# Kernel tuning notes

Measured on AMD Instinct MI355X. Metric: run time of the kernel, lower is better.

Reference implementation:

```python
import jax, jax.numpy as jnp
import numpy as np
from jax.scipy.special import i0

IM_SIZE = (256, 256)
GRID_SIZE = (512, 512)
NUMPOINTS = 6
OS = GRID_SIZE[0] / IM_SIZE[0]
# Beatty et al. optimal Kaiser-Bessel shape parameter
BETA = float(np.pi * np.sqrt((NUMPOINTS / OS) ** 2 * (OS - 0.5) ** 2 - 0.8))


def _apod_1d(N, G):
    # 1/FT(kb kernel) scaling coefficients (de-apodization), static numpy
    x = np.arange(N) - N / 2.0
    arg = np.pi * NUMPOINTS * x / G
    t = BETA ** 2 - arg ** 2  # > 0 for this config
    ph = np.sinh(np.sqrt(t)) / np.sqrt(t)
    return (1.0 / ph).astype(np.float32)


def _kb(u):
    # Kaiser-Bessel interpolation kernel, support |u| <= NUMPOINTS/2
    x = 2.0 * u / NUMPOINTS
    t = 1.0 - x * x
    inside = t > 0
    t = jnp.where(inside, t, 0.0)
    return jnp.where(inside, i0(BETA * jnp.sqrt(t)), 0.0)


def setup_inputs():
    key = jax.random.key(0)
    k1, k2, k3 = jax.random.split(key, 3)
    B, M = 8, 131072
    image = jax.random.normal(k1, (B,) + IM_SIZE, dtype=jnp.float32)
    ktraj = (jax.random.uniform(k2, (B, 2, M), dtype=jnp.float32) * 2.0 - 1.0) * jnp.pi
    dcf = jax.random.uniform(k3, (B, M), dtype=jnp.float32)
    return {"image": image, "ktraj": ktraj, "dcf": dcf}


def _nufft(image, ktraj, dcf):
    B = image.shape[0]
    N1, N2 = IM_SIZE
    G1, G2 = GRID_SIZE
    J = NUMPOINTS
    # 1) de-apodization (scaling coefficients), separable per-dim
    a1 = jnp.asarray(_apod_1d(N1, G1))
    a2 = jnp.asarray(_apod_1d(N2, G2))
    img = image.astype(jnp.complex64) * (a1[:, None] * a2[None, :])
    # 2) centered zero-pad to oversampled grid, FFT with DC at bin 0
    p1, p2 = (G1 - N1) // 2, (G2 - N2) // 2
    grid = jnp.zeros((B, G1, G2), dtype=jnp.complex64).at[:, p1:p1 + N1, p2:p2 + N2].set(img)
    kgrid = jnp.fft.fft2(jnp.fft.ifftshift(grid, axes=(1, 2)))
    # 3) KB interpolation (gather) at non-uniform points
    tm1 = ktraj[:, 0] * (G1 / (2.0 * jnp.pi))  # (B,M) in grid units
    tm2 = ktraj[:, 1] * (G2 / (2.0 * jnp.pi))
    offs = jnp.arange(J, dtype=jnp.float32) - (J // 2 - 1)  # [-2..3]
    g1 = jnp.floor(tm1)[..., None] + offs  # (B,M,J) neighbor coords
    g2 = jnp.floor(tm2)[..., None] + offs
    w1 = _kb(tm1[..., None] - g1)
    w2 = _kb(tm2[..., None] - g2)
    i1 = jnp.mod(g1.astype(jnp.int32), G1)
    i2 = jnp.mod(g2.astype(jnp.int32), G2)
    lin = (i1[..., :, None] * G2 + i2[..., None, :]).reshape(B, -1)  # (B, M*J*J)
    vals = jnp.take_along_axis(kgrid.reshape(B, -1), lin, axis=1).reshape(B, -1, J, J)
    w = (w1[..., :, None] * w2[..., None, :]).astype(jnp.complex64)
    kdata = jnp.sum(vals * w, axis=(-1, -2))  # (B,M) complex
    kdata = kdata * dcf
    return jnp.stack([kdata.real, kdata.imag], axis=0)  # (2,B,M) float32


def reference(image, ktraj, dcf):
    return _nufft(image, ktraj, dcf)
```

## Files before the change

### kernel.cpp

```cpp
#include <hip/hip_runtime.h>
#include <math.h>

#define GSZ 512
#define NSZ 256
#define NBATCH 8
#define MPTS 131072
#define PI_F 3.14159265358979f
#define BETA_F 13.8551004f
#define BETA2_F (BETA_F * BETA_F)
#define RSQ2 0.70710678f
#define PADIDX(i) ((i) + ((i) >> 3))


__device__ __forceinline__ float apod(int i) {
    float x = (float)(i - 128);
    float arg = PI_F * 6.0f * x * (1.0f / 512.0f);
    float t = BETA2_F - arg * arg;
    float st = sqrtf(t);
    return st / sinhf(st);
}

__device__ __forceinline__ float kbw(float u) {
    float t = 1.0f - u * u * (1.0f / 9.0f);
    float x = BETA_F * sqrtf(fmaxf(t, 0.0f));
    float xc = fmaxf(x, 0.35f);
    float R = __builtin_amdgcn_rsqf(xc);
    float R2 = R * R;
    float q = R * (0.39894228f + R2 * (0.04986779f + R2 * 0.02804702f));
    float w = __expf(xc) * q;
    return (t > 0.0f) ? w : 0.0f;
}

template<int CTRL>
__device__ __forceinline__ float qdpp(float v) {
    int r = __builtin_amdgcn_mov_dpp(__float_as_int(v), CTRL, 0xF, 0xF, true);
    return __int_as_float(r);
}

struct __align__(8) F4 { float x, y, z, w; };

__device__ __forceinline__ float2 cadd(float2 a, float2 b){ return make_float2(a.x+b.x, a.y+b.y); }
__device__ __forceinline__ float2 csub(float2 a, float2 b){ return make_float2(a.x-b.x, a.y-b.y); }
__device__ __forceinline__ float2 cmul(float2 a, float2 b){ return make_float2(a.x*b.x-a.y*b.y, a.x*b.y+a.y*b.x); }
__device__ __forceinline__ float2 mul_negi(float2 a){ return make_float2(a.y, -a.x); }
__device__ __forceinline__ float2 mul_posi(float2 a){ return make_float2(-a.y, a.x); }
__device__ __forceinline__ float2 mul_w81(float2 a){ return make_float2(RSQ2*(a.x+a.y), RSQ2*(a.y-a.x)); }
__device__ __forceinline__ float2 mul_w83(float2 a){ return make_float2(RSQ2*(a.y-a.x), -RSQ2*(a.x+a.y)); }

__device__ __forceinline__ void dft8_combine(float2 E0, float2 E1, float2 E2, float2 E3,
                                             float2 O0, float2 O1, float2 O2, float2 O3,
                                             float2* y) {
    float2 c1 = mul_w81(O1), c2 = mul_negi(O2), c3 = mul_w83(O3);
    y[0] = cadd(E0, O0); y[4] = csub(E0, O0);
    y[1] = cadd(E1, c1); y[5] = csub(E1, c1);
    y[2] = cadd(E2, c2); y[6] = csub(E2, c2);
    y[3] = cadd(E3, c3); y[7] = csub(E3, c3);
}

__device__ __forceinline__ void dft8(const float2* x, float2* y) {
    float2 a0=x[0], a1=x[2], a2=x[4], a3=x[6];
    float2 b0=x[1], b1=x[3], b2=x[5], b3=x[7];
    float2 ta0=cadd(a0,a2), ta1=csub(a0,a2), ta2=cadd(a1,a3), ta3=csub(a1,a3);
    float2 E0=cadd(ta0,ta2), E2=csub(ta0,ta2);
    float2 E1=cadd(ta1, mul_negi(ta3)), E3=cadd(ta1, mul_posi(ta3));
    float2 tb0=cadd(b0,b2), tb1=csub(b0,b2), tb2=cadd(b1,b3), tb3=csub(b1,b3);
    float2 O0=cadd(tb0,tb2), O2=csub(tb0,tb2);
    float2 O1=cadd(tb1, mul_negi(tb3)), O3=cadd(tb1, mul_posi(tb3));
    dft8_combine(E0,E1,E2,E3,O0,O1,O2,O3,y);
}

__device__ __forceinline__ void dft8_pruned(float2 x0, float2 x1, float2 x6, float2 x7, float2* y) {
    float2 E0 = cadd(x0, x6), E2 = csub(x0, x6);
    float2 E1 = cadd(x0, mul_posi(x6)), E3 = cadd(x0, mul_negi(x6));
    float2 O0 = cadd(x1, x7), O2 = csub(x1, x7);
    float2 O1 = cadd(x1, mul_posi(x7)), O3 = cadd(x1, mul_negi(x7));
    dft8_combine(E0,E1,E2,E3,O0,O1,O2,O3,y);
}

template<int S>
__device__ __forceinline__ void twiddle8(int t, float2* y) {
    if (S < 2) {
        int j = (S == 0) ? t : (t >> 3);
        const float scale = (S == 0) ? (-2.0f*PI_F/512.0f) : (-2.0f*PI_F/64.0f);
        float theta = scale * (float)j;
        float sn, cs;
        __sincosf(theta, &sn, &cs);
        float2 w = make_float2(cs, sn), wq = w;
        y[1] = cmul(y[1], wq);
        #pragma unroll
        for (int q = 2; q < 8; ++q) { wq = cmul(wq, w); y[q] = cmul(y[q], wq); }
    }
}

__global__ __launch_bounds__(128) void pass1_rowfft(const float* __restrict__ image,
                                                    float2* __restrict__ T) {
    __shared__ float2 sm[2][2][578];
    int tid = threadIdx.x;
    int r = tid >> 6, t = tid & 63;
    int blk = blockIdx.x;
    int p = blk & 3;
    int g = blk >> 2;
    int rp = (g << 1) + r;
    int y = (rp < 128) ? rp : (rp + 256);
    int iy = (y < 128) ? (y + 128) : (y - 384);
    float ay = apod(iy);
    const float* irow0 = image + ((size_t)((2 * p)     * NSZ + iy)) * NSZ;
    const float* irow1 = image + ((size_t)((2 * p + 1) * NSZ + iy)) * NSZ;

    float2 y8[8];
    {
        int ix0 = t + 128, ix1 = t + 192, ix6 = t, ix7 = t + 64;
        float w0 = ay * apod(ix0), w1 = ay * apod(ix1);
        float w6 = ay * apod(ix6), w7 = ay * apod(ix7);
        float2 x0 = make_float2(irow0[ix0] * w0, irow1[ix0] * w0);
        float2 x1 = make_float2(irow0[ix1] * w1, irow1[ix1] * w1);
        float2 x6 = make_float2(irow0[ix6] * w6, irow1[ix6] * w6);
        float2 x7 = make_float2(irow0[ix7] * w7, irow1[ix7] * w7);
        dft8_pruned(x0, x1, x6, x7, y8);
        twiddle8<0>(t, y8);
    }
    float2* A  = sm[0][r];
    float2* Bf = sm[1][r];
    #pragma unroll
    for (int q = 0; q < 8; ++q) A[PADIDX((t << 3) + q)] = y8[q];
    __syncthreads();
    {
        float2 x[8];
        #pragma unroll
        for (int pp = 0; pp < 8; ++pp) x[pp] = A[PADIDX(t + (pp << 6))];
        dft8(x, y8);
        twiddle8<1>(t, y8);
        int j = t >> 3, k = t & 7, base = k + (j << 6);
        #pragma unroll
        for (int q = 0; q < 8; ++q) Bf[PADIDX(base + (q << 3))] = y8[q];
    }
    __syncthreads();
    {
        float2 x[8];
        #pragma unroll
        for (int pp = 0; pp < 8; ++pp) x[pp] = Bf[PADIDX(t + (pp << 6))];
        dft8(x, y8);
        float2* Trow = T + (((size_t)(p << 8) + rp) << 9);
        #pragma unroll
        for (int q = 0; q < 8; ++q) Trow[t + (q << 6)] = y8[q];
    }
}

__global__ __launch_bounds__(256) void pass2_colfft(const float2* __restrict__ T,
                                                    float2* __restrict__ kgrid) {
    __shared__ float2 B[8][578];
    int tid = threadIdx.x;
    int blk = blockIdx.x;
    int p = blk & 3;
    int g = blk >> 2;
    const float2* Tb = T + ((size_t)p << 17);
    float2* Kb0 = kgrid + ((size_t)(2 * p) << 18);
    float2* Kb1 = Kb0 + ((size_t)1 << 18);

    #define COLG(c) ((g > 0) ? (((c) < 4) ? ((g << 2) + (c)) : (505 - (g << 2) + (c))) \
                             : (((c) < 4) ? (c) : (((c) == 7) ? 256 : (505 + (c)))))

    {
        int c = tid & 7, r0 = tid >> 3;
        int colg = COLG(c);
        #pragma unroll
        for (int k = 0; k < 8; ++k) {
            int rr = r0 + (k << 5);
            B[c][PADIDX(rr)] = Tb[((size_t)rr << 9) + colg];
        }
    }
    __syncthreads();
    int t = tid & 63;
    int c0 = tid >> 6;
    float2* Ba = B[c0];
    float2* Bb = B[c0 + 4];
    float2 ya[8], yb[8];
    {
        float2 a0 = Ba[PADIDX(t)],       a1 = Ba[PADIDX(t + 64)];
        float2 a6 = Ba[PADIDX(t + 128)], a7 = Ba[PADIDX(t + 192)];
        float2 b0 = Bb[PADIDX(t)],       b1 = Bb[PADIDX(t + 64)];
        float2 b6 = Bb[PADIDX(t + 128)], b7 = Bb[PADIDX(t + 192)];
        dft8_pruned(a0, a1, a6, a7, ya); twiddle8<0>(t, ya);
        dft8_pruned(b0, b1, b6, b7, yb); twiddle8<0>(t, yb);
    }
    __syncthreads();
    #pragma unroll
    for (int q = 0; q < 8; ++q) {
        Ba[PADIDX((t << 3) + q)] = ya[q];
        Bb[PADIDX((t << 3) + q)] = yb[q];
    }
    __syncthreads();
    {
        float2 xa[8], xb[8];
        #pragma unroll
        for (int pp = 0; pp < 8; ++pp) { xa[pp] = Ba[PADIDX(t + (pp << 6))]; xb[pp] = Bb[PADIDX(t + (pp << 6))]; }
        dft8(xa, ya); twiddle8<1>(t, ya);
        dft8(xb, yb); twiddle8<1>(t, yb);
    }
    __syncthreads();
    {
        int j = t >> 3, k = t & 7, base = k + (j << 6);
        #pragma unroll
        for (int q = 0; q < 8; ++q) {
            Ba[PADIDX(base + (q << 3))] = ya[q];
            Bb[PADIDX(base + (q << 3))] = yb[q];
        }
    }
    __syncthreads();
    {
        float2 xa[8], xb[8];
        #pragma unroll
        for (int pp = 0; pp < 8; ++pp) { xa[pp] = Ba[PADIDX(t + (pp << 6))]; xb[pp] = Bb[PADIDX(t + (pp << 6))]; }
        dft8(xa, ya);
        dft8(xb, yb);
    }
    __syncthreads();
    #pragma unroll
    for (int q = 0; q < 8; ++q) {
        Ba[PADIDX(t + (q << 6))] = ya[q];
        Bb[PADIDX(t + (q << 6))] = yb[q];
    }
    __syncthreads();
    {
        int c = tid & 7, r0 = tid >> 3;
        int colg = COLG(c);
        int mc = 7 - c;
        if (g == 0) { if (c == 0) mc = 0; else if (c == 7) mc = 7; }
        #pragma unroll
        for (int k = 0; k < 16; ++k) {
            int rr = r0 + (k << 5);
            int mr = (512 - rr) & 511;
            float2 Z = B[c][PADIDX(rr)];
            float2 M = B[mc][PADIDX(mr)];
            float2 K0 = make_float2(0.5f * (Z.x + M.x), 0.5f * (Z.y - M.y));
            float2 K1 = make_float2(0.5f * (Z.y + M.y), 0.5f * (M.x - Z.x));
            size_t off = ((size_t)rr << 9) + colg;
            Kb0[off] = K0;
            Kb1[off] = K1;
        }
    }
    #undef COLG
}

__global__ __launch_bounds__(256) void interp_kb(const float* __restrict__ ktraj,
                                                 const float* __restrict__ dcf,
                                                 const float2* __restrict__ kgrid,
                                                 float* __restrict__ out) {
    int tid = threadIdx.x;
    int blk = blockIdx.x;
    int b = blk & 7;
    int gb = blk >> 3;
    int j = tid & 3;
    int q = tid >> 2;

    const float SCALE = (float)GSZ / (2.0f * PI_F);
    const float2* Kb = kgrid + ((size_t)b << 18);
    const float* kt1 = ktraj + ((size_t)(b * 2)) * MPTS;
    const float* kt2 = kt1 + MPTS;
    const float* dcfb = dcf + ((size_t)b << 17);
    float* out_re = out + ((size_t)b << 17);
    float* out_im = out_re + (size_t)NBATCH * MPTS;

    int m0 = (gb << 9) + q;
    float tm1 = kt1[m0] * SCALE;
    float tm2 = kt2[m0] * SCALE;
    float dd  = dcfb[m0];

    #pragma unroll 2
    for (int it = 0; it < 8; ++it) {
        int m = m0 + (it << 6);
        float f1 = floorf(tm1), f2 = floorf(tm2);
        int if1 = (int)f1, if2 = (int)f2;
        int e0 = (if2 - 2) & ~1;
        int cpair = (e0 + 2 * j) & 511;

        F4 v[6];
        #pragma unroll
        for (int a = 0; a < 6; ++a) {
            int rowb = (if1 + a - 2) & 511;
            v[a] = *reinterpret_cast<const F4*>(Kb + ((size_t)rowb << 9) + cpair);
        }

        float u2 = tm2 - (float)(e0 + 2 * j);
        float w2a = kbw(u2);
        float w2b = kbw(u2 - 1.0f);
        float fr1 = tm1 - f1;
        float w1A = kbw(fr1 - (float)(j - 2));
        float w1B = kbw(fr1 - (float)(j + 2));
        float w1_[6];
        w1_[0] = qdpp<0x00>(w1A);
        w1_[1] = qdpp<0x55>(w1A);
        w1_[2] = qdpp<0xAA>(w1A);
        w1_[3] = qdpp<0xFF>(w1A);
        w1_[4] = qdpp<0x00>(w1B);
        w1_[5] = qdpp<0x55>(w1B);
        float myd = dd;

        if (it < 7) {
            int mn = m + 64;
            tm1 = kt1[mn] * SCALE;
            tm2 = kt2[mn] * SCALE;
            dd  = dcfb[mn];
        }

        float c0re = 0.f, c0im = 0.f, c1re = 0.f, c1im = 0.f;
        #pragma unroll
        for (int a = 0; a < 6; ++a) {
            c0re = fmaf(w1_[a], v[a].x, c0re); c0im = fmaf(w1_[a], v[a].y, c0im);
            c1re = fmaf(w1_[a], v[a].z, c1re); c1im = fmaf(w1_[a], v[a].w, c1im);
        }
        float p_re = fmaf(w2a, c0re, w2b * c1re);
        float p_im = fmaf(w2a, c0im, w2b * c1im);
        p_re += qdpp<0xB1>(p_re);  p_re += qdpp<0x4E>(p_re);
        p_im += qdpp<0xB1>(p_im);  p_im += qdpp<0x4E>(p_im);

        if (j == 0) out_re[m] = p_re * myd;
        if (j == 1) out_im[m] = p_im * myd;
    }
}


extern "C" void kernel_launch(void* const* d_in, const int* in_sizes, int n_in,
                              void* d_out, int out_size, void* d_ws, size_t ws_size,
                              hipStream_t stream) {
    const float* image = (const float*)d_in[0];
    const float* ktraj = (const float*)d_in[1];
    const float* dcf   = (const float*)d_in[2];
    float* out = (float*)d_out;

    float2* T     = (float2*)d_ws;
    float2* kgrid = T + (size_t)4 * 256 * GSZ;

    pass1_rowfft<<<512, 128, 0, stream>>>(image, T);
    pass2_colfft<<<256, 256, 0, stream>>>(T, kgrid);
    interp_kb<<<NBATCH * 256, 256, 0, stream>>>(ktraj, dcf, kgrid, out);
}
```

Measured before the change: 128.4 us.

## Prefetch all trajectory inputs and double-buffer grid gathers in interpolation kernel

Result: slower. 132.1 us (+2.9%).

```diff
diff --git a/kernel.cpp b/kernel.cpp
--- a/kernel.cpp
+++ b/kernel.cpp
@@ -36,8 +36,6 @@
     int r = __builtin_amdgcn_mov_dpp(__float_as_int(v), CTRL, 0xF, 0xF, true);
     return __int_as_float(r);
 }
-
-struct __align__(8) F4 { float x, y, z, w; };
 
 __device__ __forceinline__ float2 cadd(float2 a, float2 b){ return make_float2(a.x+b.x, a.y+b.y); }
 __device__ __forceinline__ float2 csub(float2 a, float2 b){ return make_float2(a.x-b.x, a.y-b.y); }
@@ -252,9 +250,10 @@
     int gb = blk >> 3;
     int j = tid & 3;
     int q = tid >> 2;
+    int j2 = j << 1;
 
     const float SCALE = (float)GSZ / (2.0f * PI_F);
-    const float2* Kb = kgrid + ((size_t)b << 18);
+    const float* Kf = (const float*)(kgrid + ((size_t)b << 18));
     const float* kt1 = ktraj + ((size_t)(b * 2)) * MPTS;
     const float* kt2 = kt1 + MPTS;
     const float* dcfb = dcf + ((size_t)b << 17);
@@ -262,26 +261,32 @@
     float* out_im = out_re + (size_t)NBATCH * MPTS;
 
     int m0 = (gb << 9) + q;
-    float tm1 = kt1[m0] * SCALE;
-    float tm2 = kt2[m0] * SCALE;
-    float dd  = dcfb[m0];
-
-    #pragma unroll 2
+
+    float r1[8], r2[8], rd[8];
+    #pragma unroll
     for (int it = 0; it < 8; ++it) {
-        int m = m0 + (it << 6);
+        int mm = m0 + (it << 6);
+        r1[it] = __builtin_nontemporal_load(&kt1[mm]);
+        r2[it] = __builtin_nontemporal_load(&kt2[mm]);
+        rd[it] = __builtin_nontemporal_load(&dcfb[mm]);
+    }
+
+    auto issue = [&](float tm1, float tm2, float4* v, float& f1s, int& e0s) {
         float f1 = floorf(tm1), f2 = floorf(tm2);
         int if1 = (int)f1, if2 = (int)f2;
         int e0 = (if2 - 2) & ~1;
-        int cpair = (e0 + 2 * j) & 511;
-
-        F4 v[6];
+        int cpair = (e0 + j2) & 511;
         #pragma unroll
         for (int a = 0; a < 6; ++a) {
             int rowb = (if1 + a - 2) & 511;
-            v[a] = *reinterpret_cast<const F4*>(Kb + ((size_t)rowb << 9) + cpair);
-        }
-
-        float u2 = tm2 - (float)(e0 + 2 * j);
+            v[a] = *reinterpret_cast<const float4*>(Kf + ((rowb << 10) + (cpair << 1)));
+        }
+        f1s = f1; e0s = e0;
+    };
+
+    auto consume = [&](float tm1, float tm2, float f1, int e0, const float4* v,
+                       float dd, int m) {
+        float u2 = tm2 - (float)(e0 + j2);
         float w2a = kbw(u2);
         float w2b = kbw(u2 - 1.0f);
         float fr1 = tm1 - f1;
@@ -294,14 +299,6 @@
         w1_[3] = qdpp<0xFF>(w1A);
         w1_[4] = qdpp<0x00>(w1B);
         w1_[5] = qdpp<0x55>(w1B);
-        float myd = dd;
-
-        if (it < 7) {
-            int mn = m + 64;
-            tm1 = kt1[mn] * SCALE;
-            tm2 = kt2[mn] * SCALE;
-            dd  = dcfb[mn];
-        }
 
         float c0re = 0.f, c0im = 0.f, c1re = 0.f, c1im = 0.f;
         #pragma unroll
@@ -314,8 +311,30 @@
         p_re += qdpp<0xB1>(p_re);  p_re += qdpp<0x4E>(p_re);
         p_im += qdpp<0xB1>(p_im);  p_im += qdpp<0x4E>(p_im);
 
-        if (j == 0) out_re[m] = p_re * myd;
-        if (j == 1) out_im[m] = p_im * myd;
+        if (j == 0) __builtin_nontemporal_store(p_re * dd, &out_re[m]);
+        if (j == 1) __builtin_nontemporal_store(p_im * dd, &out_im[m]);
+    };
+
+    float4 vA[6], vB[6];
+    float f1A, f1B; int e0A, e0B;
+    float t1A = r1[0] * SCALE, t2A = r2[0] * SCALE;
+    float t1B = r1[1] * SCALE, t2B = r2[1] * SCALE;
+    issue(t1A, t2A, vA, f1A, e0A);
+    issue(t1B, t2B, vB, f1B, e0B);
+
+    #pragma unroll
+    for (int k = 0; k < 4; ++k) {
+        int itA = 2 * k, itB = 2 * k + 1;
+        consume(t1A, t2A, f1A, e0A, vA, rd[itA], m0 + (itA << 6));
+        if (k < 3) {
+            t1A = r1[itA + 2] * SCALE; t2A = r2[itA + 2] * SCALE;
+            issue(t1A, t2A, vA, f1A, e0A);
+        }
+        consume(t1B, t2B, f1B, e0B, vB, rd[itB], m0 + (itB << 6));
+        if (k < 3) {
+            t1B = r1[itB + 2] * SCALE; t2B = r2[itB + 2] * SCALE;
+            issue(t1B, t2B, vB, f1B, e0B);
+        }
     }
 }
 
```

## Software-pipeline KB interpolation gathers with inline-asm loads and manual vmcnt waits

Applied to the files above, without the earlier changes.

New measurement: 127.8 us. About the same (-0.5%).

```diff
diff --git a/kernel.cpp b/kernel.cpp
--- a/kernel.cpp
+++ b/kernel.cpp
@@ -11,6 +11,15 @@
 #define RSQ2 0.70710678f
 #define PADIDX(i) ((i) + ((i) >> 3))
 
+typedef float f32x4 __attribute__((ext_vector_type(4)));
+
+#define GLOAD4(dst, ptr) asm volatile("global_load_dwordx4 %0, %1, off" : "=&v"(dst) : "v"(ptr) : "memory")
+#define GLOAD1(dst, ptr) asm volatile("global_load_dword %0, %1, off"   : "=&v"(dst) : "v"(ptr) : "memory")
+#define GSTORE1(val, ptr) asm volatile("global_store_dword %0, %1, off" :: "v"(ptr), "v"(val) : "memory")
+#define WAITVM(n) do { asm volatile("s_waitcnt vmcnt(" #n ")" ::: "memory"); \
+                       __builtin_amdgcn_sched_barrier(0); } while (0)
+#define SBAR() __builtin_amdgcn_sched_barrier(0)
+
 
 __device__ __forceinline__ float apod(int i) {
     float x = (float)(i - 128);
@@ -36,8 +45,6 @@
     int r = __builtin_amdgcn_mov_dpp(__float_as_int(v), CTRL, 0xF, 0xF, true);
     return __int_as_float(r);
 }
-
-struct __align__(8) F4 { float x, y, z, w; };
 
 __device__ __forceinline__ float2 cadd(float2 a, float2 b){ return make_float2(a.x+b.x, a.y+b.y); }
 __device__ __forceinline__ float2 csub(float2 a, float2 b){ return make_float2(a.x-b.x, a.y-b.y); }
@@ -242,6 +249,61 @@
     #undef COLG
 }
 
+
+#define ISSUE(i, V0, V1, V2, V3, V4, V5) do {                               \
+    float tm1 = r1v[i] * SCALE, tm2 = r2v[i] * SCALE;                       \
+    float f1 = floorf(tm1), f2 = floorf(tm2);                               \
+    int if1 = (int)f1, if2 = (int)f2;                                       \
+    int e0 = (if2 - 2) & ~1;                             \
+    int cpair = (e0 + j2) & 511;           \
+    const float* pb = Kf + (cpair << 1);                                    \
+    GLOAD4(V0, pb + (((if1 - 2) & 511) << 10));                             \
+    GLOAD4(V1, pb + (((if1 - 1) & 511) << 10));                             \
+    GLOAD4(V2, pb + (((if1    ) & 511) << 10));                             \
+    GLOAD4(V3, pb + (((if1 + 1) & 511) << 10));                             \
+    GLOAD4(V4, pb + (((if1 + 2) & 511) << 10));                             \
+    GLOAD4(V5, pb + (((if1 + 3) & 511) << 10));                             \
+    fr1v[i] = tm1 - f1;                                                     \
+    u2v[i]  = tm2 - (float)(e0 + j2);                                       \
+    SBAR();                                                                 \
+} while (0)
+
+#define WEIGHTS(i)                                                          \
+    float u2_##i  = u2v[i];                                                 \
+    float w2a_##i = kbw(u2_##i);                                            \
+    float w2b_##i = kbw(u2_##i - 1.0f);                                     \
+    float w1A_##i = kbw(fr1v[i] - fjm2);                                    \
+    float w1B_##i = kbw(fr1v[i] - fjp2);                                    \
+    float w0_##i = qdpp<0x00>(w1A_##i);                                     \
+    float w1_##i = qdpp<0x55>(w1A_##i);                                     \
+    float w2_##i = qdpp<0xAA>(w1A_##i);                                     \
+    float w3_##i = qdpp<0xFF>(w1A_##i);                                     \
+    float w4_##i = qdpp<0x00>(w1B_##i);                                     \
+    float w5_##i = qdpp<0x55>(w1B_##i);
+
+#define FMACONS(i, V0, V1, V2, V3, V4, V5) do {                             \
+    float c0re = w0_##i * V0.x, c0im = w0_##i * V0.y;                       \
+    float c1re = w0_##i * V0.z, c1im = w0_##i * V0.w;                       \
+    c0re = fmaf(w1_##i, V1.x, c0re); c0im = fmaf(w1_##i, V1.y, c0im);       \
+    c1re = fmaf(w1_##i, V1.z, c1re); c1im = fmaf(w1_##i, V1.w, c1im);       \
+    c0re = fmaf(w2_##i, V2.x, c0re); c0im = fmaf(w2_##i, V2.y, c0im);       \
+    c1re = fmaf(w2_##i, V2.z, c1re); c1im = fmaf(w2_##i, V2.w, c1im);       \
+    c0re = fmaf(w3_##i, V3.x, c0re); c0im = fmaf(w3_##i, V3.y, c0im);       \
+    c1re = fmaf(w3_##i, V3.z, c1re); c1im = fmaf(w3_##i, V3.w, c1im);       \
+    c0re = fmaf(w4_##i, V4.x, c0re); c0im = fmaf(w4_##i, V4.y, c0im);       \
+    c1re = fmaf(w4_##i, V4.z, c1re); c1im = fmaf(w4_##i, V4.w, c1im);       \
+    c0re = fmaf(w5_##i, V5.x, c0re); c0im = fmaf(w5_##i, V5.y, c0im);       \
+    c1re = fmaf(w5_##i, V5.z, c1re); c1im = fmaf(w5_##i, V5.w, c1im);       \
+    float p_re = fmaf(w2a_##i, c0re, w2b_##i * c1re);                       \
+    float p_im = fmaf(w2a_##i, c0im, w2b_##i * c1im);                       \
+    p_re += qdpp<0xB1>(p_re); p_re += qdpp<0x4E>(p_re);                     \
+    p_im += qdpp<0xB1>(p_im); p_im += qdpp<0x4E>(p_im);                     \
+    int mmm = m0 + ((i) << 6);                                              \
+    float sre = p_re * rdv[i], sim = p_im * rdv[i];                         \
+    if (j == 0) GSTORE1(sre, out_re + mmm);                                 \
+    if (j == 1) GSTORE1(sim, out_im + mmm);                                 \
+} while (0)
+
 __global__ __launch_bounds__(256) void interp_kb(const float* __restrict__ ktraj,
                                                  const float* __restrict__ dcf,
                                                  const float2* __restrict__ kgrid,
@@ -252,9 +314,11 @@
     int gb = blk >> 3;
     int j = tid & 3;
     int q = tid >> 2;
+    int j2 = j << 1;
+    float fjm2 = (float)(j - 2), fjp2 = (float)(j + 2);
 
     const float SCALE = (float)GSZ / (2.0f * PI_F);
-    const float2* Kb = kgrid + ((size_t)b << 18);
+    const float* Kf = (const float*)(kgrid + ((size_t)b << 18));
     const float* kt1 = ktraj + ((size_t)(b * 2)) * MPTS;
     const float* kt2 = kt1 + MPTS;
     const float* dcfb = dcf + ((size_t)b << 17);
@@ -262,61 +326,56 @@
     float* out_im = out_re + (size_t)NBATCH * MPTS;
 
     int m0 = (gb << 9) + q;
-    float tm1 = kt1[m0] * SCALE;
-    float tm2 = kt2[m0] * SCALE;
-    float dd  = dcfb[m0];
-
-    #pragma unroll 2
-    for (int it = 0; it < 8; ++it) {
-        int m = m0 + (it << 6);
-        float f1 = floorf(tm1), f2 = floorf(tm2);
-        int if1 = (int)f1, if2 = (int)f2;
-        int e0 = (if2 - 2) & ~1;
-        int cpair = (e0 + 2 * j) & 511;
-
-        F4 v[6];
-        #pragma unroll
-        for (int a = 0; a < 6; ++a) {
-            int rowb = (if1 + a - 2) & 511;
-            v[a] = *reinterpret_cast<const F4*>(Kb + ((size_t)rowb << 9) + cpair);
-        }
-
-        float u2 = tm2 - (float)(e0 + 2 * j);
-        float w2a = kbw(u2);
-        float w2b = kbw(u2 - 1.0f);
-        float fr1 = tm1 - f1;
-        float w1A = kbw(fr1 - (float)(j - 2));
-        float w1B = kbw(fr1 - (float)(j + 2));
-        float w1_[6];
-        w1_[0] = qdpp<0x00>(w1A);
-        w1_[1] = qdpp<0x55>(w1A);
-        w1_[2] = qdpp<0xAA>(w1A);
-        w1_[3] = qdpp<0xFF>(w1A);
-        w1_[4] = qdpp<0x00>(w1B);
-        w1_[5] = qdpp<0x55>(w1B);
-        float myd = dd;
-
-        if (it < 7) {
-            int mn = m + 64;
-            tm1 = kt1[mn] * SCALE;
-            tm2 = kt2[mn] * SCALE;
-            dd  = dcfb[mn];
-        }
-
-        float c0re = 0.f, c0im = 0.f, c1re = 0.f, c1im = 0.f;
-        #pragma unroll
-        for (int a = 0; a < 6; ++a) {
-            c0re = fmaf(w1_[a], v[a].x, c0re); c0im = fmaf(w1_[a], v[a].y, c0im);
-            c1re = fmaf(w1_[a], v[a].z, c1re); c1im = fmaf(w1_[a], v[a].w, c1im);
-        }
-        float p_re = fmaf(w2a, c0re, w2b * c1re);
-        float p_im = fmaf(w2a, c0im, w2b * c1im);
-        p_re += qdpp<0xB1>(p_re);  p_re += qdpp<0x4E>(p_re);
-        p_im += qdpp<0xB1>(p_im);  p_im += qdpp<0x4E>(p_im);
-
-        if (j == 0) out_re[m] = p_re * myd;
-        if (j == 1) out_im[m] = p_im * myd;
-    }
+
+    float r1v[8], r2v[8], rdv[8];
+    #define LOADPT(i) do {                     \
+        GLOAD1(r1v[i], kt1 + m0 + ((i) << 6)); \
+        GLOAD1(r2v[i], kt2 + m0 + ((i) << 6)); \
+        GLOAD1(rdv[i], dcfb + m0 + ((i) << 6)); } while (0)
+    LOADPT(0); LOADPT(1); LOADPT(2); LOADPT(3);
+    LOADPT(4); LOADPT(5); LOADPT(6); LOADPT(7);
+    #undef LOADPT
+    WAITVM(0);
+
+    float fr1v[8], u2v[8];
+    f32x4 A0, A1, A2, A3, A4, A5;
+    f32x4 B0, B1, B2, B3, B4, B5;
+
+    ISSUE(0, A0, A1, A2, A3, A4, A5);
+    ISSUE(1, B0, B1, B2, B3, B4, B5);
+
+    WEIGHTS(0);
+    WAITVM(6);
+    FMACONS(0, A0, A1, A2, A3, A4, A5);
+    ISSUE(2, A0, A1, A2, A3, A4, A5);
+    WEIGHTS(1);
+    WAITVM(6);
+    FMACONS(1, B0, B1, B2, B3, B4, B5);
+    ISSUE(3, B0, B1, B2, B3, B4, B5);
+    WEIGHTS(2);
+    WAITVM(6);
+    FMACONS(2, A0, A1, A2, A3, A4, A5);
+    ISSUE(4, A0, A1, A2, A3, A4, A5);
+    WEIGHTS(3);
+    WAITVM(6);
+    FMACONS(3, B0, B1, B2, B3, B4, B5);
+    ISSUE(5, B0, B1, B2, B3, B4, B5);
+    WEIGHTS(4);
+    WAITVM(6);
+    FMACONS(4, A0, A1, A2, A3, A4, A5);
+    ISSUE(6, A0, A1, A2, A3, A4, A5);
+    WEIGHTS(5);
+    WAITVM(6);
+    FMACONS(5, B0, B1, B2, B3, B4, B5);
+    ISSUE(7, B0, B1, B2, B3, B4, B5);
+    WEIGHTS(6);
+    WAITVM(6);
+    FMACONS(6, A0, A1, A2, A3, A4, A5);
+    WEIGHTS(7);
+    WAITVM(0);
+    FMACONS(7, B0, B1, B2, B3, B4, B5);
+
+    WAITVM(0);
 }
 
 
```
